# Kernel tuning notes

Measured on AMD Instinct MI355X. Metric: run time of the kernel, lower is better.

Reference implementation:

```python
import jax, jax.numpy as jnp
import numpy as np
from jax import lax

SIGMOID_THRESH = 0.05


def setup_inputs() -> dict:
    key = jax.random.key(0)
    # [B, num_kps, H, W] raw (pre-sigmoid) heatmap logits
    heatmaps = jax.random.normal(key, (16, 17, 512, 512), dtype=jnp.float32)
    return {"heatmaps": heatmaps, "kernel_size": 3}


def reference(heatmaps, kernel_size):
    # Faithful to Heatmaps.get_local_max_coords, expressed as a dense mask
    # (torch.nonzero has a data-dependent output shape, so we return the
    # masked peak scores instead of the coordinate list; the coordinate
    # extraction is a trivial host-side nonzero on the mask).
    assert kernel_size % 2 == 1
    pad = kernel_size // 2
    # max_pool2d(kernel_size, stride=1, padding=kernel_size//2)
    max_heatmaps = lax.reduce_window(
        heatmaps,
        -jnp.inf,
        lax.max,
        window_dimensions=(1, 1, kernel_size, kernel_size),
        window_strides=(1, 1, 1, 1),
        padding=((0, 0), (0, 0), (pad, pad), (pad, pad)),
    )
    scores = jax.nn.sigmoid(heatmaps)
    keep = (max_heatmaps == heatmaps) & (scores > SIGMOID_THRESH)
    # peak score map: nonzero entries are exactly the coords torch.nonzero
    # would return, with the peak confidence as the value.
    return jnp.where(keep, scores, jnp.zeros((), dtype=heatmaps.dtype))
```

## Files before the change

### kernel.cpp

```cpp
#include <hip/hip_runtime.h>
#include <math.h>

#define HM_W 512
#define HM_H 512
#define TILE_ROWS 16
#define HALO_ROWS (TILE_ROWS + 2)
#define LDS_STRIDE 516
#define SIG_THRESH 0.05f

typedef float f32x4 __attribute__((ext_vector_type(4)));

__global__ __launch_bounds__(512) void heatmap_peak_kernel(
    const float* __restrict__ in, float* __restrict__ out) {
    __shared__ float s[HALO_ROWS][LDS_STRIDE];

    const int tx = threadIdx.x;
    const int ty = threadIdx.y;
    const int t  = ty * 128 + tx;
    const int y0 = blockIdx.y * TILE_ROWS;
    const long long base = (long long)blockIdx.z * (HM_H * HM_W);

    for (int i = t; i < HALO_ROWS * 128; i += 512) {
        const int r  = i >> 7;
        const int c  = i & 127;
        const int gy = y0 - 1 + r;
        float4 v;
        if (gy >= 0 && gy < HM_H) {
            v = ((const float4*)(in + base + (long long)gy * HM_W))[c];
        } else {
            v = make_float4(-INFINITY, -INFINITY, -INFINITY, -INFINITY);
        }
        *(float4*)&s[r][c * 4] = v;
    }
    __syncthreads();

    const int x0   = tx * 4;
    const int row0 = ty * 4;
    const bool has_l = (x0 != 0);
    const bool has_r = (x0 + 4 < HM_W);

    float4 a = *(const float4*)&s[row0][x0];
    float4 b = *(const float4*)&s[row0 + 1][x0];
    float la = has_l ? s[row0][x0 - 1]     : -INFINITY;
    float lb = has_l ? s[row0 + 1][x0 - 1] : -INFINITY;
    float ra = has_r ? s[row0][x0 + 4]     : -INFINITY;
    float rb = has_r ? s[row0 + 1][x0 + 4] : -INFINITY;

    #pragma unroll
    for (int k = 0; k < 4; ++k) {
        const int rr = row0 + k;
        const float4 c4 = *(const float4*)&s[rr + 2][x0];
        const float  lc = has_l ? s[rr + 2][x0 - 1] : -INFINITY;
        const float  rc = has_r ? s[rr + 2][x0 + 4] : -INFINITY;

        float4 vm;
        vm.x = fmaxf(fmaxf(a.x, b.x), c4.x);
        vm.y = fmaxf(fmaxf(a.y, b.y), c4.y);
        vm.z = fmaxf(fmaxf(a.z, b.z), c4.z);
        vm.w = fmaxf(fmaxf(a.w, b.w), c4.w);
        const float lm = fmaxf(fmaxf(la, lb), lc);
        const float rm = fmaxf(fmaxf(ra, rb), rc);

        float4 hm;
        hm.x = fmaxf(lm,   fmaxf(vm.x, vm.y));
        hm.y = fmaxf(vm.x, fmaxf(vm.y, vm.z));
        hm.z = fmaxf(vm.y, fmaxf(vm.z, vm.w));
        hm.w = fmaxf(vm.z, fmaxf(vm.w, rm));

        f32x4 o;
        {
            const float sc = 1.0f / (1.0f + __expf(-b.x));
            o.x = (hm.x == b.x && sc > SIG_THRESH) ? sc : 0.0f;
        }
        {
            const float sc = 1.0f / (1.0f + __expf(-b.y));
            o.y = (hm.y == b.y && sc > SIG_THRESH) ? sc : 0.0f;
        }
        {
            const float sc = 1.0f / (1.0f + __expf(-b.z));
            o.z = (hm.z == b.z && sc > SIG_THRESH) ? sc : 0.0f;
        }
        {
            const float sc = 1.0f / (1.0f + __expf(-b.w));
            o.w = (hm.w == b.w && sc > SIG_THRESH) ? sc : 0.0f;
        }

        f32x4* optr = (f32x4*)(out + base + (long long)(y0 + rr) * HM_W) + tx;
        __builtin_nontemporal_store(o, optr);

        a = b; b = c4;
        la = lb; lb = lc;
        ra = rb; rb = rc;
    }
}

extern "C" void kernel_launch(void* const* d_in, const int* in_sizes, int n_in,
                              void* d_out, int out_size, void* d_ws, size_t ws_size,
                              hipStream_t stream) {
    const float* heatmaps = (const float*)d_in[0];
    float* out = (float*)d_out;

    const int planes = in_sizes[0] / (HM_H * HM_W);

    dim3 block(128, 4, 1);
    dim3 grid(1, HM_H / TILE_ROWS, planes);
    heatmap_peak_kernel<<<grid, block, 0, stream>>>(heatmaps, out);
}
```

Before: 474.7 us.

## Replace LDS tiling with per-wave vertical strip streaming and lane shuffles

Drops the shared-memory tile and has each wavefront walk a 64-row vertical strip, reading each row straight from global memory into registers. Horizontal neighbours come from cross-lane shuffles, and only the edge lanes load halo elements. This removes the LDS staging, the barrier and most of the halo re-reads across row tiles. In exchange, far fewer blocks are launched (2x2x272), which lowers parallelism, and the nontemporal stores become normal stores.

After: 479.7 us. Within noise of the previous version (+1.1%).

```diff
diff --git a/kernel.cpp b/kernel.cpp
--- a/kernel.cpp
+++ b/kernel.cpp
@@ -3,61 +3,57 @@
 
 #define HM_W 512
 #define HM_H 512
-#define TILE_ROWS 16
-#define HALO_ROWS (TILE_ROWS + 2)
-#define LDS_STRIDE 516
+#define STRIP 64
 #define SIG_THRESH 0.05f
 
-typedef float f32x4 __attribute__((ext_vector_type(4)));
+__global__ __launch_bounds__(256) void heatmap_peak_kernel(
+    const float* __restrict__ in, float* __restrict__ out) {
+    const int lane  = threadIdx.x;
+    const int chunk = blockIdx.x;
+    const int x0    = chunk * 256 + lane * 4;
+    const int ys    = blockIdx.y * (4 * STRIP) + threadIdx.y * STRIP;
+    const long long base = (long long)blockIdx.z * (long long)(HM_H * HM_W);
+    const float* plane = in + base;
 
-__global__ __launch_bounds__(512) void heatmap_peak_kernel(
-    const float* __restrict__ in, float* __restrict__ out) {
-    __shared__ float s[HALO_ROWS][LDS_STRIDE];
+    const bool lane0  = (lane == 0);
+    const bool lane63 = (lane == 63);
+    const bool need_l = lane0  && (x0 > 0);
+    const bool need_r = lane63 && (x0 + 4 < HM_W);
 
-    const int tx = threadIdx.x;
-    const int ty = threadIdx.y;
-    const int t  = ty * 128 + tx;
-    const int y0 = blockIdx.y * TILE_ROWS;
-    const long long base = (long long)blockIdx.z * (HM_H * HM_W);
-
-    for (int i = t; i < HALO_ROWS * 128; i += 512) {
-        const int r  = i >> 7;
-        const int c  = i & 127;
-        const int gy = y0 - 1 + r;
-        float4 v;
-        if (gy >= 0 && gy < HM_H) {
-            v = ((const float4*)(in + base + (long long)gy * HM_W))[c];
+    auto load_row = [&](int y, float4& v, float& l, float& r) {
+        if (y >= 0 && y < HM_H) {
+            const float* rp = plane + (long long)y * HM_W;
+            v = *(const float4*)(rp + x0);
+            const float le = need_l ? rp[x0 - 1] : -INFINITY;
+            const float re = need_r ? rp[x0 + 4] : -INFINITY;
+            l = __shfl_up(v.w, 1);
+            if (lane0) l = le;
+            r = __shfl_down(v.x, 1);
+            if (lane63) r = re;
         } else {
             v = make_float4(-INFINITY, -INFINITY, -INFINITY, -INFINITY);
+            l = -INFINITY;
+            r = -INFINITY;
         }
-        *(float4*)&s[r][c * 4] = v;
-    }
-    __syncthreads();
+    };
 
-    const int x0   = tx * 4;
-    const int row0 = ty * 4;
-    const bool has_l = (x0 != 0);
-    const bool has_r = (x0 + 4 < HM_W);
+    float4 a, b;
+    float la, lb, ra, rb;
+    load_row(ys - 1, a, la, ra);
+    load_row(ys,     b, lb, rb);
 
-    float4 a = *(const float4*)&s[row0][x0];
-    float4 b = *(const float4*)&s[row0 + 1][x0];
-    float la = has_l ? s[row0][x0 - 1]     : -INFINITY;
-    float lb = has_l ? s[row0 + 1][x0 - 1] : -INFINITY;
-    float ra = has_r ? s[row0][x0 + 4]     : -INFINITY;
-    float rb = has_r ? s[row0 + 1][x0 + 4] : -INFINITY;
-
-    #pragma unroll
-    for (int k = 0; k < 4; ++k) {
-        const int rr = row0 + k;
-        const float4 c4 = *(const float4*)&s[rr + 2][x0];
-        const float  lc = has_l ? s[rr + 2][x0 - 1] : -INFINITY;
-        const float  rc = has_r ? s[rr + 2][x0 + 4] : -INFINITY;
+    #pragma unroll 4
+    for (int k = 0; k < STRIP; ++k) {
+        const int y = ys + k;
+        float4 c;
+        float lc, rc;
+        load_row(y + 1, c, lc, rc);
 
         float4 vm;
-        vm.x = fmaxf(fmaxf(a.x, b.x), c4.x);
-        vm.y = fmaxf(fmaxf(a.y, b.y), c4.y);
-        vm.z = fmaxf(fmaxf(a.z, b.z), c4.z);
-        vm.w = fmaxf(fmaxf(a.w, b.w), c4.w);
+        vm.x = fmaxf(fmaxf(a.x, b.x), c.x);
+        vm.y = fmaxf(fmaxf(a.y, b.y), c.y);
+        vm.z = fmaxf(fmaxf(a.z, b.z), c.z);
+        vm.w = fmaxf(fmaxf(a.w, b.w), c.w);
         const float lm = fmaxf(fmaxf(la, lb), lc);
         const float rm = fmaxf(fmaxf(ra, rb), rc);
 
@@ -67,7 +63,7 @@
         hm.z = fmaxf(vm.y, fmaxf(vm.z, vm.w));
         hm.w = fmaxf(vm.z, fmaxf(vm.w, rm));
 
-        f32x4 o;
+        float4 o;
         {
             const float sc = 1.0f / (1.0f + __expf(-b.x));
             o.x = (hm.x == b.x && sc > SIG_THRESH) ? sc : 0.0f;
@@ -85,10 +81,9 @@
             o.w = (hm.w == b.w && sc > SIG_THRESH) ? sc : 0.0f;
         }
 
-        f32x4* optr = (f32x4*)(out + base + (long long)(y0 + rr) * HM_W) + tx;
-        __builtin_nontemporal_store(o, optr);
+        *(float4*)(out + base + (long long)y * HM_W + x0) = o;
 
-        a = b; b = c4;
+        a = b; b = c;
         la = lb; lb = lc;
         ra = rb; rb = rc;
     }
@@ -102,7 +97,7 @@
 
     const int planes = in_sizes[0] / (HM_H * HM_W);
 
-    dim3 block(128, 4, 1);
-    dim3 grid(1, HM_H / TILE_ROWS, planes);
+    dim3 block(64, 4, 1);
+    dim3 grid(2, HM_H / (4 * STRIP), planes);
     heatmap_peak_kernel<<<grid, block, 0, stream>>>(heatmaps, out);
 }
```
